# Kernel optimization log

Hardware: AMD Instinct MI355X
Metric: run time of the kernel (lower is better)

Reference implementation:

```python
import jax, jax.numpy as jnp
from jax import lax
import numpy as np

BN_EPS = 1e-5

def _bn(x, g, b, m, v):
    # inference-mode BatchNorm1d (running stats)
    return (x - m) * (g / jnp.sqrt(v + BN_EPS)) + b

def _mlp2(x, W1, g, b, m, v, W2):
    # Linear(no bias) -> BN -> ReLU -> (Dropout off in eval) -> Linear(no bias)
    h = jax.nn.relu(_bn(x @ W1.T, g, b, m, v))
    return h @ W2.T

def setup_inputs() -> dict:
    key = jax.random.key(0)
    ks = iter(jax.random.split(key, 40))
    B, N = 1024, 10
    f32 = jnp.float32
    def w(shape, s=0.02):
        return jax.random.normal(next(ks), shape, f32) * s
    def bn_params(c):
        return (jnp.ones((c,), f32), jnp.zeros((c,), f32),
                jax.random.normal(next(ks), (c,), f32) * 0.1,
                jax.random.uniform(next(ks), (c,), f32, 0.5, 1.5))
    inp = {
        'features_object': jax.random.normal(next(ks), (B, N, 1024), f32),
        'bbox': jax.random.uniform(next(ks), (B, N, 4), f32),
        'word_embedding': jax.random.normal(next(ks), (B, N, 300), f32),
        'sentiment': jax.random.normal(next(ks), (B, N, 4096), f32),
        'body': jax.random.normal(next(ks), (B, 2048), f32),
    }
    # mlp_object: 1024 -> 128 -> 128
    inp['W1_o'] = w((128, 1024)); inp['g_o'], inp['b_o'], inp['m_o'], inp['v_o'] = bn_params(128)
    inp['W2_o'] = w((128, 128))
    # mlp_sentiment: 4096 -> 512 -> 128
    inp['W1_s'] = w((512, 4096)); inp['g_s'], inp['b_s'], inp['m_s'], inp['v_s'] = bn_params(512)
    inp['W2_s'] = w((128, 512))
    # mlp_body: 2048 -> 256 -> 128
    inp['W1_b'] = w((256, 2048)); inp['g_b'], inp['b_b'], inp['m_b'], inp['v_b'] = bn_params(256)
    inp['W2_b'] = w((128, 256))
    # channel attention (CBAM-style, in_planes=10, ratio=2): shared MLP 10->5->10
    inp['Wc1'] = w((5, 10), 0.3)
    inp['Wc2'] = w((10, 5), 0.3)
    # spatial attention: Conv1d(2 -> 1, k=7, pad=3, no bias)
    inp['Wsa'] = w((1, 2, 7), 0.3)
    # fc1: 688 -> 256 (with bias) then BN
    inp['Wf'] = w((256, 688)); inp['bf'] = jnp.zeros((256,), f32)
    inp['g_f'], inp['b_f'], inp['m_f'], inp['v_f'] = bn_params(256)
    return inp

def reference(features_object, bbox, word_embedding, sentiment, body,
              W1_o, g_o, b_o, m_o, v_o, W2_o,
              W1_s, g_s, b_s, m_s, v_s, W2_s,
              W1_b, g_b, b_b, m_b, v_b, W2_b,
              Wc1, Wc2, Wsa, Wf, bf, g_f, b_f, m_f, v_f):
    B, N, _ = features_object.shape
    # per-slice MLPs batched into single GEMMs over B*N rows
    obj = _mlp2(features_object.reshape(B * N, -1), W1_o, g_o, b_o, m_o, v_o, W2_o).reshape(B, N, 128)
    sen = _mlp2(sentiment.reshape(B * N, -1), W1_s, g_s, b_s, m_s, v_s, W2_s).reshape(B, N, 128)
    # body is identical across the N repeats (inference BN), compute once and broadcast
    bod = _mlp2(body.reshape(B, -1), W1_b, g_b, b_b, m_b, v_b, W2_b)
    bod = jnp.broadcast_to(bod[:, None, :], (B, N, 128))
    x = jnp.concatenate([obj, bbox, word_embedding, sen, bod], axis=2)  # [B,N,688]
    # channel attention over the N-slice axis
    def ca_mlp(a):  # [B,N] -> [B,N]
        return jax.nn.relu(a @ Wc1.T) @ Wc2.T
    att_c = jax.nn.sigmoid(ca_mlp(x.mean(axis=2)) + ca_mlp(x.max(axis=2)))  # [B,N]
    x = x * att_c[:, :, None]
    # spatial attention along feature axis
    s = jnp.stack([x.mean(axis=1), x.max(axis=1)], axis=1)  # [B,2,688]
    sa = lax.conv_general_dilated(s, Wsa, (1,), [(3, 3)],
                                  dimension_numbers=('NCH', 'OIH', 'NCH'))  # [B,1,688]
    x = x * jax.nn.sigmoid(sa)
    x = x.sum(axis=1)  # [B,688]
    out = jax.nn.relu(_bn(x @ Wf.T + bf, g_f, b_f, m_f, v_f))  # [B,256]
    return out
```

## Files before the change

kernel.cpp:

```cpp
#include <hip/hip_runtime.h>
#include <hip/hip_bf16.h>
#include <math.h>

typedef __attribute__((ext_vector_type(8))) short short8;
typedef __attribute__((ext_vector_type(4))) float floatx4;

static __device__ __forceinline__ unsigned short f2bf(float f) {
    unsigned int u = __float_as_uint(f);
    unsigned int r = (u + 0x7fffu + ((u >> 16) & 1u)) >> 16;
    return (unsigned short)r;
}

static __device__ __forceinline__ void g2l16(const void* g, void* l) {
    __builtin_amdgcn_global_load_lds(
        (const __attribute__((address_space(1))) unsigned int*)g,
        (__attribute__((address_space(3))) unsigned int*)l,
        16, 0, 0);
}

struct GDesc {
    const float*          Af;
    const unsigned short* Ab;
    const unsigned short* W;
    float*          Cf;
    unsigned short* Cb;
    const float *bias, *g, *b, *m, *v;
    int M, N, K;
    int Kreal;
    int fuse;
    int nbx;
    int block0;
};
struct GArgs { GDesc g[3]; int n; };

__global__ __launch_bounds__(256)
void gemm_grouped(GArgs ga)
{
    __shared__ unsigned short As[2][4096];
    __shared__ unsigned short Bs[2][4096];

    const int bid = blockIdx.x;
    int gi = 0;
    #pragma unroll
    for (int i = 1; i < 3; ++i)
        if (i < ga.n && bid >= ga.g[i].block0) gi = i;
    const GDesc d = ga.g[gi];
    const int local = bid - d.block0;
    const int bx = local % d.nbx;
    const int by = local / d.nbx;
    const int row0 = by * 128;
    const int col0 = bx * 128;

    const int tid  = threadIdx.x;
    const int wave = tid >> 6;
    const int lane = tid & 63;
    const int qd   = lane >> 4;
    const int ln   = lane & 15;
    const int wr   = (wave >> 1) * 64;
    const int wc   = (wave & 1) * 64;

    const int c0 = wave * 128 + lane;
    const int c1 = c0 + 64;
    const int r0 = c0 >> 2, k0 = (c0 & 3) * 8;
    const int r1 = c1 >> 2, k1 = (c1 & 3) * 8;

    const int sr = tid >> 3;
    const int sc = (tid & 7) * 4;

    const bool afp = (d.Af != nullptr);
    const int niter = d.K >> 5;

    floatx4 acc[4][4];
    #pragma unroll
    for (int i = 0; i < 4; ++i)
        #pragma unroll
        for (int j = 0; j < 4; ++j) acc[i][j] = (floatx4){0.f, 0.f, 0.f, 0.f};

    g2l16(d.W + (size_t)(col0 + r0) * d.K + k0, &Bs[0][(size_t)wave * 1024]);
    g2l16(d.W + (size_t)(col0 + r1) * d.K + k1, &Bs[0][(size_t)wave * 1024 + 512]);
    if (afp) {
        #pragma unroll
        for (int p = 0; p < 4; ++p) {
            float4 v = (sc < d.Kreal)
                ? *(const float4*)(d.Af + (size_t)(row0 + p * 32 + sr) * d.Kreal + sc)
                : (float4){0.f, 0.f, 0.f, 0.f};
            ushort4 o = { f2bf(v.x), f2bf(v.y), f2bf(v.z), f2bf(v.w) };
            *(ushort4*)&As[0][(p * 32 + sr) * 32 + sc] = o;
        }
    } else {
        g2l16(d.Ab + (size_t)(row0 + r0) * d.K + k0, &As[0][(size_t)wave * 1024]);
        g2l16(d.Ab + (size_t)(row0 + r1) * d.K + k1, &As[0][(size_t)wave * 1024 + 512]);
    }
    __syncthreads();

    int cur = 0;
    for (int it = 0; it < niter; ++it) {
        const int kk = it * 32;
        const int nxt = cur ^ 1;
        const bool pf = (it + 1 < niter);

        float4 areg[4];
        if (pf) {
            const int kn = kk + 32;
            g2l16(d.W + (size_t)(col0 + r0) * d.K + kn + k0, &Bs[nxt][(size_t)wave * 1024]);
            g2l16(d.W + (size_t)(col0 + r1) * d.K + kn + k1, &Bs[nxt][(size_t)wave * 1024 + 512]);
            if (afp) {
                #pragma unroll
                for (int p = 0; p < 4; ++p)
                    areg[p] = (kn + sc < d.Kreal)
                        ? *(const float4*)(d.Af + (size_t)(row0 + p * 32 + sr) * d.Kreal + kn + sc)
                        : (float4){0.f, 0.f, 0.f, 0.f};
            } else {
                g2l16(d.Ab + (size_t)(row0 + r0) * d.K + kn + k0, &As[nxt][(size_t)wave * 1024]);
                g2l16(d.Ab + (size_t)(row0 + r1) * d.K + kn + k1, &As[nxt][(size_t)wave * 1024 + 512]);
            }
        }

        short8 a[4], b[4];
        #pragma unroll
        for (int i = 0; i < 4; ++i)
            a[i] = *(const short8*)&As[cur][(wr + i * 16 + ln) * 32 + qd * 8];
        #pragma unroll
        for (int j = 0; j < 4; ++j)
            b[j] = *(const short8*)&Bs[cur][(wc + j * 16 + ln) * 32 + qd * 8];
        #pragma unroll
        for (int i = 0; i < 4; ++i)
            #pragma unroll
            for (int j = 0; j < 4; ++j)
                acc[i][j] = __builtin_amdgcn_mfma_f32_16x16x32_bf16(
                                a[i], b[j], acc[i][j], 0, 0, 0);

        if (pf && afp) {
            #pragma unroll
            for (int p = 0; p < 4; ++p) {
                ushort4 o = { f2bf(areg[p].x), f2bf(areg[p].y),
                              f2bf(areg[p].z), f2bf(areg[p].w) };
                *(ushort4*)&As[nxt][(p * 32 + sr) * 32 + sc] = o;
            }
        }
        __syncthreads();
        cur = nxt;
    }

    #pragma unroll
    for (int j = 0; j < 4; ++j) {
        const int col = col0 + wc + j * 16 + ln;
        float add = d.bias ? d.bias[col] : 0.f;
        float scale = 1.f, shift = 0.f;
        if (d.fuse) {
            scale = d.g[col] * rsqrtf(d.v[col] + 1e-5f);
            shift = d.b[col] - d.m[col] * scale;
        }
        #pragma unroll
        for (int i = 0; i < 4; ++i) {
            #pragma unroll
            for (int r = 0; r < 4; ++r) {
                const int row = row0 + wr + i * 16 + qd * 4 + r;
                float vv = acc[i][j][r] + add;
                if (d.fuse) vv = fmaxf(vv * scale + shift, 0.f);
                if (d.Cf) d.Cf[(size_t)row * d.N + col] = vv;
                if (d.Cb) d.Cb[(size_t)row * d.N + col] = f2bf(vv);
            }
        }
    }
}

struct WSeg { const float* src; unsigned short* dst; int Kreal; int Kp; };
struct WArgs { WSeg s[7]; int off[8]; };

__global__ __launch_bounds__(256)
void cvt_weights(WArgs wa)
{
    int i = blockIdx.x * 256 + threadIdx.x;
    if (i >= wa.off[7]) return;
    int s = 0;
    #pragma unroll
    for (int j = 1; j < 7; ++j) if (i >= wa.off[j]) s = j;
    const WSeg sg = wa.s[s];
    const int li = i - wa.off[s];
    const int r = li / sg.Kp, c = li - r * sg.Kp;
    sg.dst[li] = (c < sg.Kreal) ? f2bf(sg.src[(size_t)r * sg.Kreal + c])
                                : (unsigned short)0;
}

__global__ __launch_bounds__(256)
void attn_kernel(const float* __restrict__ obj, const float* __restrict__ bbox,
                 const float* __restrict__ word, const float* __restrict__ sen,
                 const float* __restrict__ bod,
                 const float* __restrict__ Wc1, const float* __restrict__ Wc2,
                 const float* __restrict__ Wsa,
                 float* __restrict__ xsum_out)
{
    const int b = blockIdx.x;
    const int tid = threadIdx.x;

    __shared__ float xs[10][688];
    __shared__ float s0[688], s1[688];
    __shared__ float avec[10], mvec[10], att[10];
    __shared__ float cw[14], c1[50], c2[50];

    if (tid < 14) cw[tid] = Wsa[tid];
    if (tid < 50) { c1[tid] = Wc1[tid]; c2[tid] = Wc2[tid]; }

    for (int n = 0; n < 10; ++n) {
        const float* o  = obj  + ((size_t)b * 10 + n) * 128;
        const float* bx = bbox + ((size_t)b * 10 + n) * 4;
        const float* w  = word + ((size_t)b * 10 + n) * 300;
        const float* s  = sen  + ((size_t)b * 10 + n) * 128;
        const float* bo = bod  + (size_t)b * 128;
        for (int c = tid; c < 688; c += 256) {
            float v;
            if      (c < 128) v = o[c];
            else if (c < 132) v = bx[c - 128];
            else if (c < 432) v = w[c - 132];
            else if (c < 560) v = s[c - 432];
            else              v = bo[c - 560];
            xs[n][c] = v;
        }
    }
    __syncthreads();

    if (tid < 10) {
        float sm = 0.f, mx = -INFINITY;
        for (int c = 0; c < 688; ++c) {
            float v = xs[tid][c];
            sm += v; mx = fmaxf(mx, v);
        }
        avec[tid] = sm * (1.f / 688.f);
        mvec[tid] = mx;
    }
    __syncthreads();

    if (tid == 0) {
        float ha[5], hm[5];
        #pragma unroll
        for (int i = 0; i < 5; ++i) {
            float sa_ = 0.f, sm_ = 0.f;
            #pragma unroll
            for (int j = 0; j < 10; ++j) {
                sa_ += c1[i * 10 + j] * avec[j];
                sm_ += c1[i * 10 + j] * mvec[j];
            }
            ha[i] = fmaxf(sa_, 0.f);
            hm[i] = fmaxf(sm_, 0.f);
        }
        #pragma unroll
        for (int j = 0; j < 10; ++j) {
            float v = 0.f;
            #pragma unroll
            for (int i = 0; i < 5; ++i) v += c2[j * 5 + i] * (ha[i] + hm[i]);
            att[j] = 1.f / (1.f + expf(-v));
        }
    }
    __syncthreads();

    for (int c = tid; c < 688; c += 256) {
        float sm = 0.f, mx = -INFINITY;
        #pragma unroll
        for (int n = 0; n < 10; ++n) {
            float v = xs[n][c] * att[n];
            xs[n][c] = v;
            sm += v; mx = fmaxf(mx, v);
        }
        s0[c] = sm * 0.1f;
        s1[c] = mx;
    }
    __syncthreads();

    for (int c = tid; c < 688; c += 256) {
        float sa = 0.f;
        #pragma unroll
        for (int j = 0; j < 7; ++j) {
            int cc = c + j - 3;
            if (cc >= 0 && cc < 688)
                sa += cw[j] * s0[cc] + cw[7 + j] * s1[cc];
        }
        float sig = 1.f / (1.f + expf(-sa));
        float sm = 0.f;
        #pragma unroll
        for (int n = 0; n < 10; ++n) sm += xs[n][c];
        xsum_out[(size_t)b * 688 + c] = sm * sig;
    }
}

extern "C" void kernel_launch(void* const* d_in, const int* in_sizes, int n_in,
                              void* d_out, int out_size, void* d_ws, size_t ws_size,
                              hipStream_t stream)
{
    const float* f_obj = (const float*)d_in[0];
    const float* bbox  = (const float*)d_in[1];
    const float* word  = (const float*)d_in[2];
    const float* sent  = (const float*)d_in[3];
    const float* body  = (const float*)d_in[4];
    const float* W1_o  = (const float*)d_in[5];
    const float* g_o = (const float*)d_in[6],  *b_o = (const float*)d_in[7];
    const float* m_o = (const float*)d_in[8],  *v_o = (const float*)d_in[9];
    const float* W2_o  = (const float*)d_in[10];
    const float* W1_s  = (const float*)d_in[11];
    const float* g_s = (const float*)d_in[12], *b_s = (const float*)d_in[13];
    const float* m_s = (const float*)d_in[14], *v_s = (const float*)d_in[15];
    const float* W2_s  = (const float*)d_in[16];
    const float* W1_b  = (const float*)d_in[17];
    const float* g_b = (const float*)d_in[18], *b_b = (const float*)d_in[19];
    const float* m_b = (const float*)d_in[20], *v_b = (const float*)d_in[21];
    const float* W2_b  = (const float*)d_in[22];
    const float* Wc1 = (const float*)d_in[23];
    const float* Wc2 = (const float*)d_in[24];
    const float* Wsa = (const float*)d_in[25];
    const float* Wf  = (const float*)d_in[26];
    const float* bf  = (const float*)d_in[27];
    const float* g_f = (const float*)d_in[28], *b_f = (const float*)d_in[29];
    const float* m_f = (const float*)d_in[30], *v_f = (const float*)d_in[31];
    float* out = (float*)d_out;

    char* p = (char*)d_ws;
    unsigned short* w1s = (unsigned short*)p; p += 4194304;
    unsigned short* w2s = (unsigned short*)p; p += 131072;
    unsigned short* w1o = (unsigned short*)p; p += 262144;
    unsigned short* w2o = (unsigned short*)p; p += 32768;
    unsigned short* w1b = (unsigned short*)p; p += 1048576;
    unsigned short* w2b = (unsigned short*)p; p += 65536;
    unsigned short* wfp = (unsigned short*)p; p += 360448;
    unsigned short* h_s = (unsigned short*)p; p += 10485760;
    unsigned short* h_o = (unsigned short*)p; p += 2621440;
    unsigned short* h_b = (unsigned short*)p; p += 524288;
    float* sen_f  = (float*)p; p += 5242880;
    float* obj_f  = (float*)p; p += 5242880;
    float* bod_f  = (float*)p; p += 524288;
    float* xsum_f = (float*)p; p += 2818048;
    if ((size_t)(p - (char*)d_ws) > ws_size) return;

    WArgs wa;
    wa.s[0] = { W1_s, w1s, 4096, 4096 };
    wa.s[1] = { W2_s, w2s,  512,  512 };
    wa.s[2] = { W1_o, w1o, 1024, 1024 };
    wa.s[3] = { W2_o, w2o,  128,  128 };
    wa.s[4] = { W1_b, w1b, 2048, 2048 };
    wa.s[5] = { W2_b, w2b,  256,  256 };
    wa.s[6] = { Wf,   wfp,  688,  704 };
    const int wn[7] = { 512*4096, 128*512, 128*1024, 128*128, 256*2048, 128*256, 256*704 };
    wa.off[0] = 0;
    for (int i = 0; i < 7; ++i) wa.off[i + 1] = wa.off[i] + wn[i];
    cvt_weights<<<(wa.off[7] + 255) / 256, 256, 0, stream>>>(wa);

    {
        GArgs ga; ga.n = 3;
        ga.g[0] = { sent,  nullptr, w1s, nullptr, h_s, nullptr, g_s, b_s, m_s, v_s,
                    10240, 512, 4096, 4096, 1, 4, 0 };
        ga.g[1] = { f_obj, nullptr, w1o, nullptr, h_o, nullptr, g_o, b_o, m_o, v_o,
                    10240, 128, 1024, 1024, 1, 1, 320 };
        ga.g[2] = { body,  nullptr, w1b, nullptr, h_b, nullptr, g_b, b_b, m_b, v_b,
                    1024, 256, 2048, 2048, 1, 2, 400 };
        gemm_grouped<<<416, 256, 0, stream>>>(ga);
    }

    {
        GArgs ga; ga.n = 3;
        ga.g[0] = { nullptr, h_s, w2s, sen_f, nullptr, nullptr, nullptr, nullptr, nullptr, nullptr,
                    10240, 128, 512, 512, 0, 1, 0 };
        ga.g[1] = { nullptr, h_o, w2o, obj_f, nullptr, nullptr, nullptr, nullptr, nullptr, nullptr,
                    10240, 128, 128, 128, 0, 1, 80 };
        ga.g[2] = { nullptr, h_b, w2b, bod_f, nullptr, nullptr, nullptr, nullptr, nullptr, nullptr,
                    1024, 128, 256, 256, 0, 1, 160 };
        gemm_grouped<<<168, 256, 0, stream>>>(ga);
    }

    attn_kernel<<<1024, 256, 0, stream>>>(obj_f, bbox, word, sen_f, bod_f,
                                          Wc1, Wc2, Wsa, xsum_f);

    {
        GArgs ga; ga.n = 1;
        ga.g[0] = { xsum_f, nullptr, wfp, out, nullptr, bf, g_f, b_f, m_f, v_f,
                    1024, 256, 704, 688, 1, 2, 0 };
        gemm_grouped<<<16, 256, 0, stream>>>(ga);
    }
}
```

Measured before the change: 538.1 us.

## Split-K the first-layer MLP GEMMs with atomic accumulation and separate BN finalize

The first grouped GEMM now splits K in two, doubling the block count from 416 to 832 so more compute units are busy. Partial sums go by float atomicAdd into an fp32 buffer that a memset zeroes first. A new bn_finalize kernel then applies BN and ReLU and converts to bf16. In exchange it adds a large memset, atomic traffic, an fp32 round trip through memory and an extra launch.

```diff
diff --git a/kernel.cpp b/kernel.cpp
--- a/kernel.cpp
+++ b/kernel.cpp
@@ -30,6 +30,8 @@
     int fuse;
     int nbx;
     int block0;
+    int nbb;
+    int ksplit;
 };
 struct GArgs { GDesc g[3]; int n; };
 
@@ -45,7 +47,16 @@
     for (int i = 1; i < 3; ++i)
         if (i < ga.n && bid >= ga.g[i].block0) gi = i;
     const GDesc d = ga.g[gi];
-    const int local = bid - d.block0;
+
+    int local = bid - d.block0;
+    int kc = 0;
+    int Kc = d.K;
+    if (d.ksplit > 1) {
+        Kc = d.K / d.ksplit;
+        kc = local / d.nbb;
+        local -= kc * d.nbb;
+    }
+    const int kbeg = kc * Kc;
     const int bx = local % d.nbx;
     const int by = local / d.nbx;
     const int row0 = by * 128;
@@ -68,7 +79,7 @@
     const int sc = (tid & 7) * 4;
 
     const bool afp = (d.Af != nullptr);
-    const int niter = d.K >> 5;
+    const int niter = Kc >> 5;
 
     floatx4 acc[4][4];
     #pragma unroll
@@ -76,20 +87,20 @@
         #pragma unroll
         for (int j = 0; j < 4; ++j) acc[i][j] = (floatx4){0.f, 0.f, 0.f, 0.f};
 
-    g2l16(d.W + (size_t)(col0 + r0) * d.K + k0, &Bs[0][(size_t)wave * 1024]);
-    g2l16(d.W + (size_t)(col0 + r1) * d.K + k1, &Bs[0][(size_t)wave * 1024 + 512]);
+    g2l16(d.W + (size_t)(col0 + r0) * d.K + kbeg + k0, &Bs[0][(size_t)wave * 1024]);
+    g2l16(d.W + (size_t)(col0 + r1) * d.K + kbeg + k1, &Bs[0][(size_t)wave * 1024 + 512]);
     if (afp) {
         #pragma unroll
         for (int p = 0; p < 4; ++p) {
-            float4 v = (sc < d.Kreal)
-                ? *(const float4*)(d.Af + (size_t)(row0 + p * 32 + sr) * d.Kreal + sc)
+            float4 v = (kbeg + sc < d.Kreal)
+                ? *(const float4*)(d.Af + (size_t)(row0 + p * 32 + sr) * d.Kreal + kbeg + sc)
                 : (float4){0.f, 0.f, 0.f, 0.f};
             ushort4 o = { f2bf(v.x), f2bf(v.y), f2bf(v.z), f2bf(v.w) };
             *(ushort4*)&As[0][(p * 32 + sr) * 32 + sc] = o;
         }
     } else {
-        g2l16(d.Ab + (size_t)(row0 + r0) * d.K + k0, &As[0][(size_t)wave * 1024]);
-        g2l16(d.Ab + (size_t)(row0 + r1) * d.K + k1, &As[0][(size_t)wave * 1024 + 512]);
+        g2l16(d.Ab + (size_t)(row0 + r0) * d.K + kbeg + k0, &As[0][(size_t)wave * 1024]);
+        g2l16(d.Ab + (size_t)(row0 + r1) * d.K + kbeg + k1, &As[0][(size_t)wave * 1024 + 512]);
     }
     __syncthreads();
 
@@ -101,18 +112,18 @@
 
         float4 areg[4];
         if (pf) {
-            const int kn = kk + 32;
-            g2l16(d.W + (size_t)(col0 + r0) * d.K + kn + k0, &Bs[nxt][(size_t)wave * 1024]);
-            g2l16(d.W + (size_t)(col0 + r1) * d.K + kn + k1, &Bs[nxt][(size_t)wave * 1024 + 512]);
+            const int kg = kbeg + kk + 32;
+            g2l16(d.W + (size_t)(col0 + r0) * d.K + kg + k0, &Bs[nxt][(size_t)wave * 1024]);
+            g2l16(d.W + (size_t)(col0 + r1) * d.K + kg + k1, &Bs[nxt][(size_t)wave * 1024 + 512]);
             if (afp) {
                 #pragma unroll
                 for (int p = 0; p < 4; ++p)
-                    areg[p] = (kn + sc < d.Kreal)
-                        ? *(const float4*)(d.Af + (size_t)(row0 + p * 32 + sr) * d.Kreal + kn + sc)
+                    areg[p] = (kg + sc < d.Kreal)
+                        ? *(const float4*)(d.Af + (size_t)(row0 + p * 32 + sr) * d.Kreal + kg + sc)
                         : (float4){0.f, 0.f, 0.f, 0.f};
             } else {
-                g2l16(d.Ab + (size_t)(row0 + r0) * d.K + kn + k0, &As[nxt][(size_t)wave * 1024]);
-                g2l16(d.Ab + (size_t)(row0 + r1) * d.K + kn + k1, &As[nxt][(size_t)wave * 1024 + 512]);
+                g2l16(d.Ab + (size_t)(row0 + r0) * d.K + kg + k0, &As[nxt][(size_t)wave * 1024]);
+                g2l16(d.Ab + (size_t)(row0 + r1) * d.K + kg + k1, &As[nxt][(size_t)wave * 1024 + 512]);
             }
         }
 
@@ -140,6 +151,22 @@
         }
         __syncthreads();
         cur = nxt;
+    }
+
+    if (d.ksplit > 1) {
+        #pragma unroll
+        for (int j = 0; j < 4; ++j) {
+            const int col = col0 + wc + j * 16 + ln;
+            #pragma unroll
+            for (int i = 0; i < 4; ++i) {
+                #pragma unroll
+                for (int r = 0; r < 4; ++r) {
+                    const int row = row0 + wr + i * 16 + qd * 4 + r;
+                    atomicAdd(&d.Cf[(size_t)row * d.N + col], acc[i][j][r]);
+                }
+            }
+        }
+        return;
     }
 
     #pragma unroll
@@ -181,6 +208,34 @@
     const int r = li / sg.Kp, c = li - r * sg.Kp;
     sg.dst[li] = (c < sg.Kreal) ? f2bf(sg.src[(size_t)r * sg.Kreal + c])
                                 : (unsigned short)0;
+}
+
+struct FSeg { const float* src; unsigned short* dst;
+              const float *g, *b, *m, *v; int N; };
+struct FArgs { FSeg s[3]; int off[4]; };
+
+__global__ __launch_bounds__(256)
+void bn_finalize(FArgs fa)
+{
+    int i = blockIdx.x * 256 + threadIdx.x;
+    if (i >= fa.off[3]) return;
+    int s = 0;
+    #pragma unroll
+    for (int j = 1; j < 3; ++j) if (i >= fa.off[j]) s = j;
+    const FSeg sg = fa.s[s];
+    const int li = i - fa.off[s];
+    const int e = li * 4;
+    const int col = e % sg.N;
+    float4 vv = *(const float4*)(sg.src + e);
+    ushort4 o;
+    #pragma unroll
+    for (int r = 0; r < 4; ++r) {
+        float sc = sg.g[col + r] * rsqrtf(sg.v[col + r] + 1e-5f);
+        float sh = sg.b[col + r] - sg.m[col + r] * sc;
+        float x  = fmaxf((&vv.x)[r] * sc + sh, 0.f);
+        ((unsigned short*)&o)[r] = f2bf(x);
+    }
+    *(ushort4*)(sg.dst + e) = o;
 }
 
 __global__ __launch_bounds__(256)
@@ -324,11 +379,17 @@
     unsigned short* h_s = (unsigned short*)p; p += 10485760;
     unsigned short* h_o = (unsigned short*)p; p += 2621440;
     unsigned short* h_b = (unsigned short*)p; p += 524288;
-    float* sen_f  = (float*)p; p += 5242880;
-    float* obj_f  = (float*)p; p += 5242880;
-    float* bod_f  = (float*)p; p += 524288;
-    float* xsum_f = (float*)p; p += 2818048;
+    char* region = p; p += 27262976;
+    float* ps = (float*)region;
+    float* po = (float*)(region + 20971520);
+    float* pb = (float*)(region + 26214400);
+    float* sen_f  = (float*)region;
+    float* obj_f  = (float*)(region + 5242880);
+    float* bod_f  = (float*)(region + 10485760);
+    float* xsum_f = (float*)(region + 11010048);
     if ((size_t)(p - (char*)d_ws) > ws_size) return;
+
+    hipMemsetAsync(region, 0, 27262976, stream);
 
     WArgs wa;
     wa.s[0] = { W1_s, w1s, 4096, 4096 };
@@ -345,23 +406,35 @@
 
     {
         GArgs ga; ga.n = 3;
-        ga.g[0] = { sent,  nullptr, w1s, nullptr, h_s, nullptr, g_s, b_s, m_s, v_s,
-                    10240, 512, 4096, 4096, 1, 4, 0 };
-        ga.g[1] = { f_obj, nullptr, w1o, nullptr, h_o, nullptr, g_o, b_o, m_o, v_o,
-                    10240, 128, 1024, 1024, 1, 1, 320 };
-        ga.g[2] = { body,  nullptr, w1b, nullptr, h_b, nullptr, g_b, b_b, m_b, v_b,
-                    1024, 256, 2048, 2048, 1, 2, 400 };
-        gemm_grouped<<<416, 256, 0, stream>>>(ga);
+        ga.g[0] = { sent,  nullptr, w1s, ps, nullptr, nullptr, nullptr, nullptr, nullptr, nullptr,
+                    10240, 512, 4096, 4096, 0, 4, 0,   320, 2 };
+        ga.g[1] = { f_obj, nullptr, w1o, po, nullptr, nullptr, nullptr, nullptr, nullptr, nullptr,
+                    10240, 128, 1024, 1024, 0, 1, 640, 80,  2 };
+        ga.g[2] = { body,  nullptr, w1b, pb, nullptr, nullptr, nullptr, nullptr, nullptr, nullptr,
+                    1024,  256, 2048, 2048, 0, 2, 800, 16,  2 };
+        gemm_grouped<<<832, 256, 0, stream>>>(ga);
+    }
+
+    {
+        FArgs fa;
+        fa.s[0] = { ps, h_s, g_s, b_s, m_s, v_s, 512 };
+        fa.s[1] = { po, h_o, g_o, b_o, m_o, v_o, 128 };
+        fa.s[2] = { pb, h_b, g_b, b_b, m_b, v_b, 256 };
+        fa.off[0] = 0;
+        fa.off[1] = 10240 * 512 / 4;
+        fa.off[2] = fa.off[1] + 10240 * 128 / 4;
+        fa.off[3] = fa.off[2] + 1024 * 256 / 4;
+        bn_finalize<<<(fa.off[3] + 255) / 256, 256, 0, stream>>>(fa);
     }
 
     {
         GArgs ga; ga.n = 3;
         ga.g[0] = { nullptr, h_s, w2s, sen_f, nullptr, nullptr, nullptr, nullptr, nullptr, nullptr,
-                    10240, 128, 512, 512, 0, 1, 0 };
+                    10240, 128, 512, 512, 0, 1, 0,   80, 1 };
         ga.g[1] = { nullptr, h_o, w2o, obj_f, nullptr, nullptr, nullptr, nullptr, nullptr, nullptr,
-                    10240, 128, 128, 128, 0, 1, 80 };
+                    10240, 128, 128, 128, 0, 1, 80,  80, 1 };
         ga.g[2] = { nullptr, h_b, w2b, bod_f, nullptr, nullptr, nullptr, nullptr, nullptr, nullptr,
-                    1024, 128, 256, 256, 0, 1, 160 };
+                    1024,  128, 256, 256, 0, 1, 160, 8,  1 };
         gemm_grouped<<<168, 256, 0, stream>>>(ga);
     }
 
@@ -371,7 +444,7 @@
     {
         GArgs ga; ga.n = 1;
         ga.g[0] = { xsum_f, nullptr, wfp, out, nullptr, bf, g_f, b_f, m_f, v_f,
-                    1024, 256, 704, 688, 1, 2, 0 };
+                    1024, 256, 704, 688, 1, 2, 0, 16, 1 };
         gemm_grouped<<<16, 256, 0, stream>>>(ga);
     }
 }
```

New measurement: 528.2 us. Within noise of the previous version (-1.8%).
